# Optimization experiments

Hardware: AMD Instinct MI355X
Metric: run time of the kernel (lower is better)

The kernel has to match this reference:

```python
import jax, jax.numpy as jnp
import numpy as np

B, T, D_MODEL, N_HEADS = 2, 2048, 2048, 16
HEAD_DIM = D_MODEL // N_HEADS
SCALE = HEAD_DIM ** -0.5
ROPE_THETA = 10000.0


def setup_inputs() -> dict:
    key = jax.random.key(0)
    ks = jax.random.split(key, 5)
    std = D_MODEL ** -0.5
    return {
        "x": jax.random.normal(ks[0], (B, T, D_MODEL), dtype=jnp.float32),
        "Wq": jax.random.normal(ks[1], (D_MODEL, D_MODEL), dtype=jnp.float32) * std,
        "Wk": jax.random.normal(ks[2], (D_MODEL, D_MODEL), dtype=jnp.float32) * std,
        "Wv": jax.random.normal(ks[3], (D_MODEL, D_MODEL), dtype=jnp.float32) * std,
        "Wo": jax.random.normal(ks[4], (D_MODEL, D_MODEL), dtype=jnp.float32) * std,
    }


def _rope_cos_sin(t, dtype):
    inv_freq = 1.0 / (ROPE_THETA ** (jnp.arange(0, HEAD_DIM, 2, dtype=jnp.float32) / HEAD_DIM))
    freqs = jnp.arange(t, dtype=jnp.float32)[:, None] * inv_freq[None, :]  # (T, hd/2)
    emb = jnp.concatenate([freqs, freqs], axis=-1)  # (T, hd)
    return jnp.cos(emb).astype(dtype), jnp.sin(emb).astype(dtype)


def _rotate_half(x):
    x1, x2 = jnp.split(x, 2, axis=-1)
    return jnp.concatenate([-x2, x1], axis=-1)


def _apply_rope(q, k):
    # q, k: (B, H, T, hd)
    cos, sin = _rope_cos_sin(q.shape[2], q.dtype)
    cos = cos[None, None]  # (1,1,T,hd)
    sin = sin[None, None]
    q = q * cos + _rotate_half(q) * sin
    k = k * cos + _rotate_half(k) * sin
    return q, k


def reference(x, Wq, Wk, Wv, Wo):
    b, t, _ = x.shape
    # projections (nn.Linear: x @ W.T), split heads: b t (h d) -> b h t d
    def proj(W):
        return jnp.einsum('btm,nm->btn', x, W).reshape(b, t, N_HEADS, HEAD_DIM).transpose(0, 2, 1, 3)
    Q, K, V = proj(Wq), proj(Wk), proj(Wv)
    Q, K = _apply_rope(Q, K)
    scores = jnp.einsum('bhtd,bhsd->bhts', Q, K) * SCALE  # (B,H,T,T)
    causal_mask = jnp.tril(jnp.ones((t, t), dtype=bool))
    scores = jnp.where(causal_mask[None, None], scores, -jnp.inf)
    attn = jax.nn.softmax(scores, axis=-1)
    attn = jnp.nan_to_num(attn, nan=0.0)
    out = jnp.einsum('bhts,bhsd->bhtd', attn, V)
    out = out.transpose(0, 2, 1, 3).reshape(b, t, D_MODEL)
    return jnp.einsum('btm,nm->btn', out, Wo)
```

## Files before the change

kernel.cpp:

```cpp
#include <hip/hip_runtime.h>

typedef unsigned short ushort_t;
typedef short bf16x8 __attribute__((ext_vector_type(8)));
typedef float f32x4 __attribute__((ext_vector_type(4)));

#define D_MODEL 2048
#define T_SEQ 2048
#define NB 2
#define NH 16
#define HD 128
#define M_ROWS 4096

__device__ __forceinline__ float b2f(unsigned short u) {
    return __uint_as_float(((unsigned)u) << 16);
}
__device__ __forceinline__ unsigned short f2b(float f) {
    unsigned u = __float_as_uint(f);
    u += 0x7fffu + ((u >> 16) & 1u);
    return (unsigned short)(u >> 16);
}

__device__ __forceinline__ void g2l16(const ushort_t* g, ushort_t* l) {
    __builtin_amdgcn_global_load_lds(
        (const __attribute__((address_space(1))) unsigned int*)g,
        (__attribute__((address_space(3))) unsigned int*)l, 16, 0, 0);
}

__global__ void detect_dtype(const ushort_t* __restrict__ x, int* __restrict__ flag) {
    __shared__ int cnt;
    if (threadIdx.x == 0) cnt = 0;
    __syncthreads();
    int c = 0;
    for (int i = threadIdx.x; i < 8192; i += 256) {
        int e = (x[i] >> 7) & 0xFF;
        if (e >= 0xC8) ++c;
    }
    atomicAdd(&cnt, c);
    __syncthreads();
    if (threadIdx.x == 0) *flag = (cnt > 16) ? 1 : 0;
}

__global__ void convert_in(const void* __restrict__ src, ushort_t* __restrict__ dst,
                           int n, const int* __restrict__ flag) {
    int i = (blockIdx.x * 256 + threadIdx.x) * 8;
    if (i >= n) return;
    if (*flag) {
        const float* s = (const float*)src;
        union { ushort_t u[8]; float4 f; } pk;
        #pragma unroll
        for (int j = 0; j < 8; ++j) pk.u[j] = f2b(s[i + j]);
        *(float4*)(dst + i) = pk.f;
    } else {
        *(float4*)(dst + i) = *(const float4*)((const ushort_t*)src + i);
    }
}

__global__ void rope_table(float* __restrict__ tab) {
    int tid = blockIdx.x * 256 + threadIdx.x;
    int i = tid & 63, t = tid >> 6;
    float ang = (float)t * exp2f(-(float)i * 0.20762050593046015f);
    tab[t * 128 + i]      = cosf(ang);
    tab[t * 128 + 64 + i] = sinf(ang);
}

__global__ __launch_bounds__(256) void gemm_nt(const ushort_t* __restrict__ A,
                                               const ushort_t* __restrict__ W,
                                               ushort_t* __restrict__ C,
                                               float* __restrict__ outf,
                                               const int* __restrict__ flag,
                                               const float* __restrict__ rtab,
                                               int mode, int Kdim, int Ndim) {
    __shared__ ushort_t smem[2 * 128 * 64];
    ushort_t* As = smem;
    ushort_t* Ws = smem + 128 * 64;
    const int tid  = threadIdx.x;
    const int lane = tid & 63;
    const int w    = tid >> 6;
    const int wr   = (w >> 1) * 64, wc = (w & 1) * 64;
    const int quad = lane >> 4, l16 = lane & 15;
    const long bm = (long)blockIdx.y * 128;
    const long bn = (long)blockIdx.x * 128;

    f32x4 acc[4][4];
    for (int i = 0; i < 4; ++i)
        for (int j = 0; j < 4; ++j) acc[i][j] = {0.f, 0.f, 0.f, 0.f};

    const int ck0 = w * 256 + lane;
    const int sw = l16 & 7;

    for (int kb = 0; kb < Kdim; kb += 64) {
        #pragma unroll
        for (int i = 0; i < 4; ++i) {
            int ck = ck0 + i * 64;
            int r = ck >> 3, g8 = (ck & 7) ^ (r & 7);
            g2l16(A + (bm + r) * Kdim + kb + g8 * 8, As + (size_t)(w * 256 + i * 64) * 8);
            g2l16(W + (bn + r) * Kdim + kb + g8 * 8, Ws + (size_t)(w * 256 + i * 64) * 8);
        }
        __syncthreads();
        #pragma unroll
        for (int kk = 0; kk < 64; kk += 32) {
            const int gb = kk >> 3;
            bf16x8 af[4], bf[4];
            #pragma unroll
            for (int i = 0; i < 4; ++i)
                af[i] = *(const bf16x8*)(As + (wr + i * 16 + l16) * 64 + ((gb + quad) ^ sw) * 8);
            #pragma unroll
            for (int j = 0; j < 4; ++j)
                bf[j] = *(const bf16x8*)(Ws + (wc + j * 16 + l16) * 64 + ((gb + quad) ^ sw) * 8);
            #pragma unroll
            for (int i = 0; i < 4; ++i)
                #pragma unroll
                for (int j = 0; j < 4; ++j)
                    acc[i][j] = __builtin_amdgcn_mfma_f32_16x16x32_bf16(af[i], bf[j], acc[i][j], 0, 0, 0);
        }
        __syncthreads();
    }

    if (mode == 2) {
        #pragma unroll
        for (int i = 0; i < 4; ++i)
            #pragma unroll
            for (int j = 0; j < 4; ++j)
                #pragma unroll
                for (int r = 0; r < 4; ++r) {
                    int row = wr + i * 16 + quad * 4 + r;
                    int col = wc + j * 16 + l16;
                    smem[col * 128 + ((((row >> 3) ^ (col & 7)) << 3) | (row & 7))] =
                        f2b(acc[i][j][r]);
                }
        __syncthreads();
        const int b = (int)(bm >> 11), t0 = (int)(bm & 2047), h = (int)(bn >> 7);
        const size_t obase = ((size_t)(b * NH + h) * HD) * T_SEQ;
        #pragma unroll
        for (int it = 0; it < 8; ++it) {
            int dd = it * 16 + (tid >> 4);
            int tch = tid & 15;
            bf16x8 v = *(const bf16x8*)(smem + dd * 128 + ((tch ^ (dd & 7)) << 3));
            *(bf16x8*)(C + obase + (size_t)dd * T_SEQ + t0 + tch * 8) = v;
        }
        return;
    }

    const int as_f32 = (outf != nullptr) && (*flag != 0);
    if (!as_f32) {
        #pragma unroll
        for (int i = 0; i < 4; ++i)
            #pragma unroll
            for (int j = 0; j < 4; ++j)
                #pragma unroll
                for (int r = 0; r < 4; ++r) {
                    int row = wr + i * 16 + quad * 4 + r;
                    int col = wc + j * 16 + l16;
                    int ch = col >> 3, off = col & 7;
                    smem[row * 128 + (((ch ^ (row & 7)) << 3) | off)] = f2b(acc[i][j][r]);
                }
        __syncthreads();
        if (mode == 1) {
            #pragma unroll
            for (int it = 0; it < 8; ++it) {
                int row = it * 16 + (tid >> 4);
                int ch  = tid & 15;
                int t = (int)((bm + row) & 2047);
                bf16x8 v = *(const bf16x8*)(smem + row * 128 + ((ch ^ (row & 7)) << 3));
                bf16x8 p = *(const bf16x8*)(smem + row * 128 + (((ch ^ 8) ^ (row & 7)) << 3));
                const float* cr = rtab + t * 128 + (ch & 7) * 8;
                float sgn = (ch < 8) ? -1.f : 1.f;
                union { ushort_t u[8]; float4 f[1]; } o;
                #pragma unroll
                for (int j = 0; j < 8; ++j) {
                    float cv = cr[j], sv = cr[64 + j];
                    o.u[j] = f2b(b2f(((const ushort_t*)&v)[j]) * cv +
                                 sgn * b2f(((const ushort_t*)&p)[j]) * sv);
                }
                *(bf16x8*)(C + (bm + row) * Ndim + bn + ch * 8) = *(const bf16x8*)o.u;
            }
        } else {
            #pragma unroll
            for (int it = 0; it < 8; ++it) {
                int row = it * 16 + (tid >> 4);
                int ch  = tid & 15;
                bf16x8 v = *(const bf16x8*)(smem + row * 128 + ((ch ^ (row & 7)) << 3));
                *(bf16x8*)(C + (bm + row) * Ndim + bn + ch * 8) = v;
            }
        }
    } else {
        float* Fs = (float*)smem;
        #pragma unroll
        for (int half = 0; half < 2; ++half) {
            __syncthreads();
            if ((w >> 1) == half) {
                #pragma unroll
                for (int i = 0; i < 4; ++i)
                    #pragma unroll
                    for (int j = 0; j < 4; ++j)
                        #pragma unroll
                        for (int r = 0; r < 4; ++r) {
                            int lr = i * 16 + quad * 4 + r;
                            int col = wc + j * 16 + l16;
                            int ch = col >> 2, off = col & 3;
                            Fs[lr * 128 + (((ch ^ (lr & 7)) << 2) | off)] = acc[i][j][r];
                        }
            }
            __syncthreads();
            #pragma unroll
            for (int it = 0; it < 8; ++it) {
                int lr = it * 8 + (tid >> 5);
                int ch = tid & 31;
                float4 v = *(const float4*)(Fs + lr * 128 + ((ch ^ (lr & 7)) << 2));
                *(float4*)(outf + (bm + half * 64 + lr) * Ndim + bn + ch * 4) = v;
            }
        }
    }
}

#define NQT (T_SEQ / 64)
#define C2SM 0.1275174452f
#define MFIX 96.0f

__global__ __launch_bounds__(256, 4) void attn_kernel(const ushort_t* __restrict__ Q,
                                                      const ushort_t* __restrict__ K,
                                                      const ushort_t* __restrict__ Vt,
                                                      ushort_t* __restrict__ O) {
    __shared__ ushort_t Ks[64 * 128];
    __shared__ ushort_t Vs[128 * 64];
    __shared__ ushort_t Ps[4 * 16 * 64];

    const int tid = threadIdx.x;
    const int lane = tid & 63, w = tid >> 6;
    const int quad = lane >> 4, l16 = lane & 15;
    const int bx = blockIdx.x;
    const int qb = (NQT - 1) - (bx >> 5);
    const int bh = bx & 31;
    const int h = bh & 15, b = bh >> 4;

    const size_t qkbase = ((size_t)(b * T_SEQ)) * D_MODEL + h * HD;
    const size_t vtbase = ((size_t)((b * NH + h) * HD)) * T_SEQ;
    const int ck0 = w * 256 + lane;
    ushort_t* Pw = Ps + w * 1024;

    auto stage_K = [&](int kvb) {
        #pragma unroll
        for (int i = 0; i < 4; ++i) {
            int ck = ck0 + i * 64;
            int r = ck >> 4, g = (ck & 15) ^ (r & 15);
            g2l16(K + qkbase + (size_t)(kvb * 64 + r) * D_MODEL + g * 8,
                  (ushort_t*)Ks + (size_t)(w * 256 + i * 64) * 8);
        }
    };
    auto stage_V = [&](int kvb) {
        #pragma unroll
        for (int i = 0; i < 4; ++i) {
            int ck = ck0 + i * 64;
            int r = ck >> 3, g = (ck & 7) ^ (r & 7);
            g2l16(Vt + vtbase + (size_t)r * T_SEQ + kvb * 64 + g * 8,
                  (ushort_t*)Vs + (size_t)(w * 256 + i * 64) * 8);
        }
    };

    bf16x8 qf[4];
    {
        const ushort_t* qrow = Q + qkbase + (size_t)(qb * 64 + w * 16 + l16) * D_MODEL;
        #pragma unroll
        for (int ks = 0; ks < 4; ++ks)
            qf[ks] = *(const bf16x8*)(qrow + ks * 32 + quad * 8);
    }

    float l_i[4] = {0.f, 0.f, 0.f, 0.f};
    f32x4 accO[8];
    for (int i = 0; i < 8; ++i) accO[i] = {0.f, 0.f, 0.f, 0.f};

    stage_K(0);

    for (int kvb = 0; kvb <= qb; ++kvb) {
        __syncthreads();
        stage_V(kvb);

        f32x4 accS[4];
        for (int i = 0; i < 4; ++i) accS[i] = {0.f, 0.f, 0.f, 0.f};
        __builtin_amdgcn_s_setprio(1);
        #pragma unroll
        for (int ks = 0; ks < 4; ++ks) {
            #pragma unroll
            for (int ct = 0; ct < 4; ++ct) {
                bf16x8 bb = *(const bf16x8*)(Ks + (ct * 16 + l16) * 128 +
                                             (((ks * 4 + quad) ^ l16) * 8));
                accS[ct] = __builtin_amdgcn_mfma_f32_16x16x32_bf16(qf[ks], bb, accS[ct], 0, 0, 0);
            }
        }
        __builtin_amdgcn_s_setprio(0);

        if (kvb == qb) {
            int qloc = w * 16 + quad * 4;
            for (int ct = 0; ct < 4; ++ct) {
                int key = ct * 16 + l16;
                for (int r = 0; r < 4; ++r)
                    if (key > qloc + r) accS[ct][r] = -1e30f;
            }
        }

        #pragma unroll
        for (int ct = 0; ct < 4; ++ct) {
            #pragma unroll
            for (int r = 0; r < 4; ++r) {
                float pv = exp2f((accS[ct][r] - MFIX) * C2SM);
                l_i[r] += pv;
                int col = ct * 16 + l16;
                int row = quad * 4 + r;
                Pw[row * 64 + ((((col >> 3) ^ (row & 7)) << 3) | (col & 7))] = f2b(pv);
            }
        }

        __syncthreads();
        if (kvb < qb) stage_K(kvb + 1);

        __builtin_amdgcn_s_setprio(1);
        #pragma unroll
        for (int kk2 = 0; kk2 < 2; ++kk2) {
            bf16x8 a = *(const bf16x8*)(Pw + l16 * 64 + (((kk2 * 4 + quad) ^ (l16 & 7)) << 3));
            #pragma unroll
            for (int ct = 0; ct < 8; ++ct) {
                bf16x8 bb = *(const bf16x8*)(Vs + (ct * 16 + l16) * 64 +
                                             (((kk2 * 4 + quad) ^ (l16 & 7)) * 8));
                accO[ct] = __builtin_amdgcn_mfma_f32_16x16x32_bf16(a, bb, accO[ct], 0, 0, 0);
            }
        }
        __builtin_amdgcn_s_setprio(0);
    }

    #pragma unroll
    for (int r = 0; r < 4; ++r) {
        for (int off = 1; off < 16; off <<= 1)
            l_i[r] += __shfl_xor(l_i[r], off);
        l_i[r] = 1.f / l_i[r];
    }

    for (int ct = 0; ct < 8; ++ct)
        for (int r = 0; r < 4; ++r) {
            size_t row = (size_t)(b * T_SEQ + qb * 64 + w * 16 + quad * 4 + r);
            O[row * D_MODEL + h * HD + ct * 16 + l16] = f2b(accO[ct][r] * l_i[r]);
        }
}

extern "C" void kernel_launch(void* const* d_in, const int* in_sizes, int n_in,
                              void* d_out, int out_size, void* d_ws, size_t ws_size,
                              hipStream_t stream) {
    const size_t TEN = (size_t)M_ROWS * D_MODEL;
    const size_t WEL = (size_t)D_MODEL * D_MODEL;

    char* ws = (char*)d_ws;
    int* flag = (int*)ws;
    ushort_t* xb  = (ushort_t*)(ws + 256);
    ushort_t* Wqb = xb  + TEN;
    ushort_t* Wkb = Wqb + WEL;
    ushort_t* Wvb = Wkb + WEL;
    ushort_t* Wob = Wvb + WEL;
    ushort_t* Qb  = Wob + WEL;
    ushort_t* Kb  = Qb + TEN;
    ushort_t* attn = Kb + TEN;
    ushort_t* Vt  = attn + TEN;
    float* rtab = (float*)(Vt + TEN);

    detect_dtype<<<1, 256, 0, stream>>>((const ushort_t*)d_in[0], flag);
    rope_table<<<(T_SEQ * 64) / 256, 256, 0, stream>>>(rtab);
    convert_in<<<(int)(TEN / 8 / 256), 256, 0, stream>>>(d_in[0], xb,  (int)TEN, flag);
    convert_in<<<(int)(WEL / 8 / 256), 256, 0, stream>>>(d_in[1], Wqb, (int)WEL, flag);
    convert_in<<<(int)(WEL / 8 / 256), 256, 0, stream>>>(d_in[2], Wkb, (int)WEL, flag);
    convert_in<<<(int)(WEL / 8 / 256), 256, 0, stream>>>(d_in[3], Wvb, (int)WEL, flag);
    convert_in<<<(int)(WEL / 8 / 256), 256, 0, stream>>>(d_in[4], Wob, (int)WEL, flag);

    dim3 gg(D_MODEL / 128, M_ROWS / 128);
    gemm_nt<<<gg, 256, 0, stream>>>(xb, Wqb, Qb, nullptr, flag, rtab, 1, D_MODEL, D_MODEL);
    gemm_nt<<<gg, 256, 0, stream>>>(xb, Wkb, Kb, nullptr, flag, rtab, 1, D_MODEL, D_MODEL);
    gemm_nt<<<gg, 256, 0, stream>>>(xb, Wvb, Vt, nullptr, flag, rtab, 2, D_MODEL, D_MODEL);
    attn_kernel<<<dim3(NQT * NB * NH), 256, 0, stream>>>(Qb, Kb, Vt, attn);
    gemm_nt<<<gg, 256, 0, stream>>>(attn, Wob, (ushort_t*)d_out, (float*)d_out, flag,
                                    rtab, 0, D_MODEL, D_MODEL);
}
```

Before: 411.2 us.

## Double-buffer GEMM LDS tiles, swizzle workgroup order, and fuse input conversions

The GEMM kernel now uses two LDS buffers, so the global-to-LDS loads for the next K tile are issued before the MFMA work on the current tile. This is meant to hide load latency behind compute. Workgroup IDs are remapped in groups of 8 to change tile traversal order and improve L2 reuse. The five separate input-conversion launches are merged into one kernel that picks its source by offset. The trade-off is that LDS per block doubles to 64KB, which may limit occupancy.

```diff
diff --git a/kernel.cpp b/kernel.cpp
--- a/kernel.cpp
+++ b/kernel.cpp
@@ -40,18 +40,31 @@
     if (threadIdx.x == 0) *flag = (cnt > 16) ? 1 : 0;
 }
 
-__global__ void convert_in(const void* __restrict__ src, ushort_t* __restrict__ dst,
-                           int n, const int* __restrict__ flag) {
-    int i = (blockIdx.x * 256 + threadIdx.x) * 8;
-    if (i >= n) return;
+__global__ void convert_all(const void* __restrict__ s0, const void* __restrict__ s1,
+                            const void* __restrict__ s2, const void* __restrict__ s3,
+                            const void* __restrict__ s4, ushort_t* __restrict__ dst,
+                            const int* __restrict__ flag) {
+    const size_t TENc = (size_t)M_ROWS * D_MODEL;
+    const size_t WELc = (size_t)D_MODEL * D_MODEL;
+    size_t i = ((size_t)blockIdx.x * 256 + threadIdx.x) * 8;
+    const void* src;
+    size_t off;
+    if (i < TENc) {
+        src = s0; off = i;
+    } else {
+        size_t j = i - TENc;
+        int wsel = (int)(j >> 22);
+        src = (wsel == 0) ? s1 : (wsel == 1) ? s2 : (wsel == 2) ? s3 : s4;
+        off = j & (WELc - 1);
+    }
     if (*flag) {
-        const float* s = (const float*)src;
+        const float* s = (const float*)src + off;
         union { ushort_t u[8]; float4 f; } pk;
         #pragma unroll
-        for (int j = 0; j < 8; ++j) pk.u[j] = f2b(s[i + j]);
+        for (int j2 = 0; j2 < 8; ++j2) pk.u[j2] = f2b(s[j2]);
         *(float4*)(dst + i) = pk.f;
     } else {
-        *(float4*)(dst + i) = *(const float4*)((const ushort_t*)src + i);
+        *(float4*)(dst + i) = *(const float4*)((const ushort_t*)src + off);
     }
 }
 
@@ -62,6 +75,8 @@
     tab[t * 128 + i]      = cosf(ang);
     tab[t * 128 + 64 + i] = sinf(ang);
 }
+
+#define SBUF (2 * 128 * 64)
 
 __global__ __launch_bounds__(256) void gemm_nt(const ushort_t* __restrict__ A,
                                                const ushort_t* __restrict__ W,
@@ -70,16 +85,18 @@
                                                const int* __restrict__ flag,
                                                const float* __restrict__ rtab,
                                                int mode, int Kdim, int Ndim) {
-    __shared__ ushort_t smem[2 * 128 * 64];
-    ushort_t* As = smem;
-    ushort_t* Ws = smem + 128 * 64;
+    __shared__ ushort_t smem[2 * SBUF];
     const int tid  = threadIdx.x;
     const int lane = tid & 63;
     const int w    = tid >> 6;
     const int wr   = (w >> 1) * 64, wc = (w & 1) * 64;
     const int quad = lane >> 4, l16 = lane & 15;
-    const long bm = (long)blockIdx.y * 128;
-    const long bn = (long)blockIdx.x * 128;
+
+    const int nwg = gridDim.x * gridDim.y;
+    const int wg  = blockIdx.y * gridDim.x + blockIdx.x;
+    const int swz = (wg & 7) * (nwg >> 3) + (wg >> 3);
+    const long bm = (long)(swz / gridDim.x) * 128;
+    const long bn = (long)(swz % gridDim.x) * 128;
 
     f32x4 acc[4][4];
     for (int i = 0; i < 4; ++i)
@@ -88,7 +105,9 @@
     const int ck0 = w * 256 + lane;
     const int sw = l16 & 7;
 
-    for (int kb = 0; kb < Kdim; kb += 64) {
+    auto stage = [&](int kb, int buf) {
+        ushort_t* As = smem + buf * SBUF;
+        ushort_t* Ws = As + 128 * 64;
         #pragma unroll
         for (int i = 0; i < 4; ++i) {
             int ck = ck0 + i * 64;
@@ -96,7 +115,15 @@
             g2l16(A + (bm + r) * Kdim + kb + g8 * 8, As + (size_t)(w * 256 + i * 64) * 8);
             g2l16(W + (bn + r) * Kdim + kb + g8 * 8, Ws + (size_t)(w * 256 + i * 64) * 8);
         }
-        __syncthreads();
+    };
+
+    stage(0, 0);
+    __syncthreads();
+    int cur = 0;
+    for (int kb = 0; kb < Kdim; kb += 64) {
+        if (kb + 64 < Kdim) stage(kb + 64, cur ^ 1);
+        const ushort_t* As = smem + cur * SBUF;
+        const ushort_t* Ws = As + 128 * 64;
         #pragma unroll
         for (int kk = 0; kk < 64; kk += 32) {
             const int gb = kk >> 3;
@@ -114,6 +141,7 @@
                     acc[i][j] = __builtin_amdgcn_mfma_f32_16x16x32_bf16(af[i], bf[j], acc[i][j], 0, 0, 0);
         }
         __syncthreads();
+        cur ^= 1;
     }
 
     if (mode == 2) {
@@ -362,11 +390,8 @@
 
     detect_dtype<<<1, 256, 0, stream>>>((const ushort_t*)d_in[0], flag);
     rope_table<<<(T_SEQ * 64) / 256, 256, 0, stream>>>(rtab);
-    convert_in<<<(int)(TEN / 8 / 256), 256, 0, stream>>>(d_in[0], xb,  (int)TEN, flag);
-    convert_in<<<(int)(WEL / 8 / 256), 256, 0, stream>>>(d_in[1], Wqb, (int)WEL, flag);
-    convert_in<<<(int)(WEL / 8 / 256), 256, 0, stream>>>(d_in[2], Wkb, (int)WEL, flag);
-    convert_in<<<(int)(WEL / 8 / 256), 256, 0, stream>>>(d_in[3], Wvb, (int)WEL, flag);
-    convert_in<<<(int)(WEL / 8 / 256), 256, 0, stream>>>(d_in[4], Wob, (int)WEL, flag);
+    convert_all<<<(int)((TEN + 4 * WEL) / 8 / 256), 256, 0, stream>>>(
+        d_in[0], d_in[1], d_in[2], d_in[3], d_in[4], xb, flag);
 
     dim3 gg(D_MODEL / 128, M_ROWS / 128);
     gemm_nt<<<gg, 256, 0, stream>>>(xb, Wqb, Qb, nullptr, flag, rtab, 1, D_MODEL, D_MODEL);
```

Result: faster. 378.7 us (-7.9%).
